# Performance work log

Hardware: AMD Instinct MI355X
Metric: run time of the kernel (lower is better)

The kernel has to match this reference:

```python
import jax, jax.numpy as jnp
import numpy as np

B, T, I, H = 64, 1024, 256, 256

def setup_inputs() -> dict:
    key = jax.random.key(0)
    ks = jax.random.split(key, 7)
    inputs = jax.random.normal(ks[0], (B * T, I), jnp.float32)
    states = jax.random.normal(ks[1], (B, 1, H), jnp.float32)  # [B, num_layers, H]
    mask = (jax.random.uniform(ks[2], (B, T, 1, 1)) < 0.9).astype(jnp.float32)
    s = 1.0 / np.sqrt(H)  # PyTorch RNN init scale
    W_ih = jax.random.uniform(ks[3], (3 * H, I), jnp.float32, -s, s)
    W_hh = jax.random.uniform(ks[4], (3 * H, H), jnp.float32, -s, s)
    b_ih = jax.random.uniform(ks[5], (3 * H,), jnp.float32, -s, s)
    b_hh = jax.random.uniform(ks[6], (3 * H,), jnp.float32, -s, s)
    return dict(inputs=inputs, states=states, mask=mask,
                W_ih=W_ih, W_hh=W_hh, b_ih=b_ih, b_hh=b_hh, seq_len=T)

def reference(inputs, states, mask, W_ih, W_hh, b_ih, b_hh, seq_len):
    # inputs: [B*T, I] -> [B, T, I]
    x = inputs.reshape(-1, seq_len, inputs.shape[-1])
    m = mask[..., 0, 0]                      # [B, T]
    # pre-loop blend: hs = states * mask[:, 0]
    h0 = states[:, 0, :] * m[:, 0:1]         # [B, H]
    xs = jnp.swapaxes(x, 0, 1)               # [T, B, I]
    ms = jnp.swapaxes(m, 0, 1)[..., None]    # [T, B, 1]

    def step(h, xm):
        x_t, m_t = xm
        gi = x_t @ W_ih.T + b_ih             # [B, 3H]
        gh = h @ W_hh.T + b_hh               # [B, 3H]
        ir, iz, i_n = jnp.split(gi, 3, axis=-1)
        hr, hz, h_n = jnp.split(gh, 3, axis=-1)
        r = jax.nn.sigmoid(ir + hr)
        z = jax.nn.sigmoid(iz + hz)
        n = jnp.tanh(i_n + r * h_n)
        nh = (1.0 - z) * n + z * h           # GRU new hidden = step output
        h_new = h * (1.0 - m_t) + nh * m_t   # masked state blend
        return h_new, nh

    h_fin, ys = jax.lax.scan(step, h0, (xs, ms))
    x_out = jnp.swapaxes(ys, 0, 1).reshape(-1, ys.shape[-1])  # [B*T, H]
    state_out = h_fin[:, None, :]                              # [B, 1, H]
    return (x_out, state_out)
```

## Files before the change

kernel.cpp:

```cpp
#include <hip/hip_runtime.h>

typedef unsigned int u32;
typedef unsigned long long u64;
typedef __fp16 f16;
typedef __fp16 h2 __attribute__((ext_vector_type(2)));
typedef __fp16 h8 __attribute__((ext_vector_type(8)));
typedef float f32x2v __attribute__((ext_vector_type(2)));
typedef float f32x4v __attribute__((ext_vector_type(4)));
typedef float f32x16v __attribute__((ext_vector_type(16)));
typedef u32 u32x2v __attribute__((ext_vector_type(2)));
typedef u32 u32x4v __attribute__((ext_vector_type(4)));

static constexpr int BB = 64;
static constexpr int TT = 1024;
static constexpr int HH = 256;
static constexpr int GG = 768;
static constexpr size_t GI_BYTES = (size_t)BB * TT * GG * 2;

__device__ __forceinline__ u32 pk2(float a, float b) {
  h2 r = __builtin_amdgcn_cvt_pkrtz(a, b);
  return __builtin_bit_cast(u32, r);
}
__device__ __forceinline__ float dpp_x1(float x) {
  return __builtin_bit_cast(float,
      __builtin_amdgcn_mov_dpp(__builtin_bit_cast(int, x), 0xB1, 0xF, 0xF, true));
}
__device__ __forceinline__ float sigf(float x) { return 1.f / (1.f + __expf(-x)); }
__device__ __forceinline__ float tanhf2(float x) {
  float e = __expf(2.f * x);
  return 1.f - 2.f / (e + 1.f);
}

__global__ void prepack_whh(const float* __restrict__ Whh, u32* __restrict__ Wp2) {
  int id = blockIdx.x * 256 + threadIdx.x;
  int j = id / 192;
  int rem = id - j * 192;
  int G = rem >> 6, d = rem & 63;
  int u = j >> 1, kh = j & 1;
  const float* p = Whh + (size_t)(G * 256 + u) * HH + 128 * kh + 2 * d;
  Wp2[id] = pk2(p[0], p[1]);
}

__device__ __forceinline__ f32x16v zero16() {
  f32x16v z;
#pragma unroll
  for (int i = 0; i < 16; ++i) z[i] = 0.f;
  return z;
}

__global__ __launch_bounds__(256, 2) void gemm_gi(
    const float* __restrict__ x, const float* __restrict__ Wih,
    const float* __restrict__ bih, const float* __restrict__ bhh,
    f16* __restrict__ gi) {
  __shared__ u32 bl[16384];
  const int tid = threadIdx.x;
  const int lane = tid & 63;
  const int wv = tid >> 6;
  const int wr = wv >> 1, wc = wv & 1;
  const int l31 = lane & 31, lh = lane >> 5;
  const int m0 = blockIdx.x << 7;

  u32x4v afr[2][16];
#pragma unroll
  for (int fr = 0; fr < 2; ++fr) {
#pragma unroll
    for (int km = 0; km < 16; ++km) {
      int row = m0 + wr * 64 + fr * 32 + l31;
      int k0 = km * 16 + lh * 8;
      const f32x4v* p = (const f32x4v*)(x + (size_t)row * 256 + k0);
      f32x4v u = p[0], v = p[1];
      u32x4v t;
      t.x = pk2(u.x, u.y); t.y = pk2(u.z, u.w);
      t.z = pk2(v.x, v.y); t.w = pk2(v.z, v.w);
      afr[fr][km] = t;
    }
  }

  for (int nt = 0; nt < 6; ++nt) {
    const int n0 = nt << 7;
#pragma unroll
    for (int it = 0; it < 32; ++it) {
      int flat = it * 256 + tid;
      int r = flat >> 6;
      int q = flat & 63;
      f32x4v f = *(const f32x4v*)(Wih + (size_t)(n0 + r) * 256 + 4 * q);
      u32x2v pw;
      pw.x = pk2(f.x, f.y);
      pw.y = pk2(f.z, f.w);
      int wd = 2 * q;
      *(u32x2v*)&bl[r * 128 + (wd ^ ((r & 15) << 2))] = pw;
    }
    __syncthreads();

    f32x16v acc00 = zero16(), acc01 = zero16(), acc10 = zero16(), acc11 = zero16();
#pragma unroll
    for (int km = 0; km < 16; ++km) {
      int w0 = km * 8 + lh * 4;
      int rc0 = wc * 64 + l31;
      int rc1 = wc * 64 + 32 + l31;
      u32x4v b0 = *(const u32x4v*)&bl[rc0 * 128 + (w0 ^ ((rc0 & 15) << 2))];
      u32x4v b1 = *(const u32x4v*)&bl[rc1 * 128 + (w0 ^ ((rc1 & 15) << 2))];
      h8 a0h = __builtin_bit_cast(h8, afr[0][km]);
      h8 a1h = __builtin_bit_cast(h8, afr[1][km]);
      h8 b0h = __builtin_bit_cast(h8, b0);
      h8 b1h = __builtin_bit_cast(h8, b1);
      acc00 = __builtin_amdgcn_mfma_f32_32x32x16_f16(a0h, b0h, acc00, 0, 0, 0);
      acc10 = __builtin_amdgcn_mfma_f32_32x32x16_f16(a1h, b0h, acc10, 0, 0, 0);
      acc01 = __builtin_amdgcn_mfma_f32_32x32x16_f16(a0h, b1h, acc01, 0, 0, 0);
      acc11 = __builtin_amdgcn_mfma_f32_32x32x16_f16(a1h, b1h, acc11, 0, 0, 0);
    }

#define EPI(ACC, FR, FC)                                                      \
    {                                                                         \
      int gc = n0 + wc * 64 + (FC) * 32 + l31;                                \
      float bias = bih[gc] + (gc < 512 ? bhh[gc] : 0.f);                      \
      _Pragma("unroll")                                                       \
      for (int rg = 0; rg < 16; ++rg) {                                       \
        int gr = m0 + wr * 64 + (FR) * 32 + 4 * lh + (rg & 3) + 8 * (rg >> 2);\
        gi[(size_t)gr * 768 + gc] = (f16)(ACC[rg] + bias);                    \
      }                                                                       \
    }
    EPI(acc00, 0, 0) EPI(acc10, 1, 0) EPI(acc01, 0, 1) EPI(acc11, 1, 1)
#undef EPI
    __syncthreads();
  }
}

#define WCLOB_LD \
  "v64","v65","v66","v67","v68","v69","v70","v71", \
  "v72","v73","v74","v75","v76","v77","v78","v79", \
  "v80","v81","v82","v83","v84","v85","v86","v87", \
  "v88","v89","v90","v91","v92","v93","v94","v95", \
  "v96","v97","v98","v99","v100","v101","v102","v103", \
  "v104","v105","v106","v107","v108","v109","v110","v111", \
  "v112","v113","v114","v115","v116","v117","v118","v119", \
  "v120","v121","v122","v123","v124","v125","v126","v127", \
  "v128","v129","v130","v131","v132","v133","v134","v135", \
  "v136","v137","v138","v139","v140","v141","v142","v143", \
  "v144","v145","v146","v147","v148","v149","v150","v151", \
  "v152","v153","v154","v155","v156","v157","v158","v159", \
  "v160","v161","v162","v163","v164","v165","v166","v167", \
  "v168","v169","v170","v171","v172","v173","v174","v175", \
  "v176","v177","v178","v179","v180","v181","v182","v183", \
  "v184","v185","v186","v187","v188","v189","v190","v191", \
  "v192","v193","v194","v195","v196","v197","v198","v199", \
  "v200","v201","v202","v203","v204","v205","v206","v207", \
  "v208","v209","v210","v211","v212","v213","v214","v215", \
  "v216","v217","v218","v219","v220","v221","v222","v223", \
  "v224","v225","v226","v227","v228","v229","v230","v231", \
  "v232","v233","v234","v235","v236","v237","v238","v239", \
  "v240","v241","v242","v243","v244","v245","v246","v247", \
  "v248","v249","v250","v251","v252","v253","v254","v255"

#define WCLOB "v56","v57","v58","v59","v60","v61","v62","v63", WCLOB_LD

#define LD16(A,B,OFF) "global_load_dwordx4 v[" #A ":" #B "], %0, off offset:" #OFF "\n\t"

#define RD_A(OFF) "ds_read_b128 v[56:59], %3 offset:" #OFF "\n\t"
#define RD_B(OFF) "ds_read_b128 v[60:63], %3 offset:" #OFF "\n\t"
#define WT1 "s_waitcnt lgkmcnt(1)\n\t"
#define WT0 "s_waitcnt lgkmcnt(0)\n\t"

#define GRP(Q0,Q1,Q2,Q3, R0,R1,R2,R3, Z0,Z1,Z2,Z3, N0,N1,N2,N3) \
  "v_dot2_f32_f16 %0, v" #R0 ", v" #Q0 ", %0\n\t" \
  "v_dot2_f32_f16 %1, v" #Z0 ", v" #Q0 ", %1\n\t" \
  "v_dot2_f32_f16 %2, v" #N0 ", v" #Q0 ", %2\n\t" \
  "v_dot2_f32_f16 %0, v" #R1 ", v" #Q1 ", %0\n\t" \
  "v_dot2_f32_f16 %1, v" #Z1 ", v" #Q1 ", %1\n\t" \
  "v_dot2_f32_f16 %2, v" #N1 ", v" #Q1 ", %2\n\t" \
  "v_dot2_f32_f16 %0, v" #R2 ", v" #Q2 ", %0\n\t" \
  "v_dot2_f32_f16 %1, v" #Z2 ", v" #Q2 ", %1\n\t" \
  "v_dot2_f32_f16 %2, v" #N2 ", v" #Q2 ", %2\n\t" \
  "v_dot2_f32_f16 %0, v" #R3 ", v" #Q3 ", %0\n\t" \
  "v_dot2_f32_f16 %1, v" #Z3 ", v" #Q3 ", %1\n\t" \
  "v_dot2_f32_f16 %2, v" #N3 ", v" #Q3 ", %2\n\t"

__global__ __launch_bounds__(512, 2) void recur(
    const u32* __restrict__ Wp2, const f16* __restrict__ gi,
    const float* __restrict__ states, const float* __restrict__ mask,
    const float* __restrict__ bhh_g, float* __restrict__ out) {
  const int b = blockIdx.x;
  const int j = threadIdx.x;
  const int u = j >> 1;
  const int kh = j & 1;

  __shared__ __align__(16) u32 hbuf[2][128];
  __shared__ float mlds[TT];

  const float bhn = bhh_g[512 + u];

  const float* mk = mask + b * TT;
  const f16* gcur = gi + (size_t)b * TT * GG + u;
  float* outb = out + (size_t)b * TT * HH;

  for (int i = j; i < TT; i += 512) mlds[i] = mk[i];

  float hreg = states[b * HH + u] * mk[0];
  if (kh == 0) ((f16*)hbuf[0])[u] = (f16)hreg;

  {
    u64 wa = (u64)(Wp2 + (size_t)j * 192);
    asm volatile(
      LD16(64,67,0)    LD16(68,71,16)   LD16(72,75,32)   LD16(76,79,48)
      LD16(80,83,64)   LD16(84,87,80)   LD16(88,91,96)   LD16(92,95,112)
      LD16(96,99,128)  LD16(100,103,144) LD16(104,107,160) LD16(108,111,176)
      LD16(112,115,192) LD16(116,119,208) LD16(120,123,224) LD16(124,127,240)
      LD16(128,131,256) LD16(132,135,272) LD16(136,139,288) LD16(140,143,304)
      LD16(144,147,320) LD16(148,151,336) LD16(152,155,352) LD16(156,159,368)
      LD16(160,163,384) LD16(164,167,400) LD16(168,171,416) LD16(172,175,432)
      LD16(176,179,448) LD16(180,183,464) LD16(184,187,480) LD16(188,191,496)
      LD16(192,195,512) LD16(196,199,528) LD16(200,203,544) LD16(204,207,560)
      LD16(208,211,576) LD16(212,215,592) LD16(216,219,608) LD16(220,223,624)
      LD16(224,227,640) LD16(228,231,656) LD16(232,235,672) LD16(236,239,688)
      LD16(240,243,704) LD16(244,247,720) LD16(248,251,736) LD16(252,255,752)
      "s_waitcnt vmcnt(0)\n\t"
      :: "v"(wa) : WCLOB_LD, "memory");
  }
  __syncthreads();

  float nh_prev = 0.f;

  for (int t = 0; t < TT; ++t) {
    if (t > 0 && kh == 0) outb[(size_t)(t - 1) * HH + u] = nh_prev;
    f16 gr_c = gcur[0], gz_c = gcur[256], gn_c = gcur[512];

    u32 lds_addr = (u32)(size_t)(&hbuf[t & 1][kh << 6]);
    float ar = 0.f, az = 0.f, an = 0.f;

    asm volatile(
      WT0
      RD_A(0) RD_B(16)
      WT1 GRP(56,57,58,59,  64,65,66,67,    128,129,130,131, 192,193,194,195) RD_A(32)
      WT1 GRP(60,61,62,63,  68,69,70,71,    132,133,134,135, 196,197,198,199) RD_B(48)
      WT1 GRP(56,57,58,59,  72,73,74,75,    136,137,138,139, 200,201,202,203) RD_A(64)
      WT1 GRP(60,61,62,63,  76,77,78,79,    140,141,142,143, 204,205,206,207) RD_B(80)
      WT1 GRP(56,57,58,59,  80,81,82,83,    144,145,146,147, 208,209,210,211) RD_A(96)
      WT1 GRP(60,61,62,63,  84,85,86,87,    148,149,150,151, 212,213,214,215) RD_B(112)
      WT1 GRP(56,57,58,59,  88,89,90,91,    152,153,154,155, 216,217,218,219) RD_A(128)
      WT1 GRP(60,61,62,63,  92,93,94,95,    156,157,158,159, 220,221,222,223) RD_B(144)
      WT1 GRP(56,57,58,59,  96,97,98,99,    160,161,162,163, 224,225,226,227) RD_A(160)
      WT1 GRP(60,61,62,63,  100,101,102,103, 164,165,166,167, 228,229,230,231) RD_B(176)
      WT1 GRP(56,57,58,59,  104,105,106,107, 168,169,170,171, 232,233,234,235) RD_A(192)
      WT1 GRP(60,61,62,63,  108,109,110,111, 172,173,174,175, 236,237,238,239) RD_B(208)
      WT1 GRP(56,57,58,59,  112,113,114,115, 176,177,178,179, 240,241,242,243) RD_A(224)
      WT1 GRP(60,61,62,63,  116,117,118,119, 180,181,182,183, 244,245,246,247) RD_B(240)
      WT1 GRP(56,57,58,59,  120,121,122,123, 184,185,186,187, 248,249,250,251)
      WT0 GRP(60,61,62,63,  124,125,126,127, 188,189,190,191, 252,253,254,255)
      : "+v"(ar), "+v"(az), "+v"(an)
      : "v"(lds_addr)
      : WCLOB, "memory");

    const float mt = mlds[t];

    float ghr = ar + dpp_x1(ar);
    float ghz = az + dpp_x1(az);
    float ghn = an + dpp_x1(an);

    float r = sigf((float)gr_c + ghr);
    float z = sigf((float)gz_c + ghz);
    float n = tanhf2((float)gn_c + r * (ghn + bhn));
    float nh = z * (hreg - n) + n;
    float hnew = hreg + mt * (nh - hreg);
    nh_prev = nh;
    hreg = hnew;
    if (kh == 0) ((f16*)hbuf[(t + 1) & 1])[u] = (f16)hnew;
    gcur += GG;
    __syncthreads();
  }

  if (kh == 0) {
    outb[(size_t)(TT - 1) * HH + u] = nh_prev;
    out[(size_t)BB * TT * HH + b * HH + u] = hreg;
  }
}

extern "C" void kernel_launch(void* const* d_in, const int* in_sizes, int n_in,
                              void* d_out, int out_size, void* d_ws, size_t ws_size,
                              hipStream_t stream) {
  const float* x      = (const float*)d_in[0];
  const float* states = (const float*)d_in[1];
  const float* mask   = (const float*)d_in[2];
  const float* W_ih   = (const float*)d_in[3];
  const float* W_hh   = (const float*)d_in[4];
  const float* b_ih   = (const float*)d_in[5];
  const float* b_hh   = (const float*)d_in[6];
  float* out = (float*)d_out;

  char* ws = (char*)d_ws;
  f16* gi = (f16*)ws;
  u32* Wp2 = (u32*)(ws + GI_BYTES);

  prepack_whh<<<dim3(384), dim3(256), 0, stream>>>(W_hh, Wp2);
  gemm_gi<<<dim3(512), dim3(256), 0, stream>>>(x, W_ih, b_ih, b_hh, gi);
  recur<<<dim3(64), dim3(512), 0, stream>>>(Wp2, gi, states, mask, b_hh, out);
}
```

Before: 1.298 ms.

## Remap GRU recurrence so each thread computes two rows over a quarter of K

The recurrent kernel now assigns each thread two hidden units and a quarter of the K dimension, instead of one unit and half of K. Each hidden-state value read from LDS then feeds six dot products rather than three, halving LDS reads per FLOP, and four read buffers are kept in flight. The hidden buffer is padded per K-chunk to avoid bank conflicts, and W_hh is prepacked to match the new layout. The cost is a two-step DPP reduction across four lanes and duplicated gate math per thread.

```diff
diff --git a/kernel.cpp b/kernel.cpp
--- a/kernel.cpp
+++ b/kernel.cpp
@@ -25,6 +25,15 @@
   return __builtin_bit_cast(float,
       __builtin_amdgcn_mov_dpp(__builtin_bit_cast(int, x), 0xB1, 0xF, 0xF, true));
 }
+__device__ __forceinline__ float dpp_x2(float x) {
+  return __builtin_bit_cast(float,
+      __builtin_amdgcn_mov_dpp(__builtin_bit_cast(int, x), 0x4E, 0xF, 0xF, true));
+}
+__device__ __forceinline__ float qred(float x) {
+  x += dpp_x1(x);
+  x += dpp_x2(x);
+  return x;
+}
 __device__ __forceinline__ float sigf(float x) { return 1.f / (1.f + __expf(-x)); }
 __device__ __forceinline__ float tanhf2(float x) {
   float e = __expf(2.f * x);
@@ -34,10 +43,16 @@
 __global__ void prepack_whh(const float* __restrict__ Whh, u32* __restrict__ Wp2) {
   int id = blockIdx.x * 256 + threadIdx.x;
   int j = id / 192;
-  int rem = id - j * 192;
-  int G = rem >> 6, d = rem & 63;
-  int u = j >> 1, kh = j & 1;
-  const float* p = Whh + (size_t)(G * 256 + u) * HH + 128 * kh + 2 * d;
+  int i = id - j * 192;
+  int m = i / 24;
+  int r24 = i - m * 24;
+  int e = r24 / 6;
+  int rs = r24 - e * 6;
+  int G = rs >> 1, uu = rs & 1;
+  int rg = j >> 2, kc = j & 3;
+  int row = G * 256 + 2 * rg + uu;
+  int k = 64 * kc + 8 * m + 2 * e;
+  const float* p = Whh + (size_t)row * HH + k;
   Wp2[id] = pk2(p[0], p[1]);
 }
 
@@ -152,28 +167,28 @@
   "v240","v241","v242","v243","v244","v245","v246","v247", \
   "v248","v249","v250","v251","v252","v253","v254","v255"
 
-#define WCLOB "v56","v57","v58","v59","v60","v61","v62","v63", WCLOB_LD
+#define WCLOB \
+  "v48","v49","v50","v51","v52","v53","v54","v55", \
+  "v56","v57","v58","v59","v60","v61","v62","v63", WCLOB_LD
 
 #define LD16(A,B,OFF) "global_load_dwordx4 v[" #A ":" #B "], %0, off offset:" #OFF "\n\t"
 
-#define RD_A(OFF) "ds_read_b128 v[56:59], %3 offset:" #OFF "\n\t"
-#define RD_B(OFF) "ds_read_b128 v[60:63], %3 offset:" #OFF "\n\t"
+#define RD0(OFF) "ds_read_b128 v[48:51], %6 offset:" #OFF "\n\t"
+#define RD1(OFF) "ds_read_b128 v[52:55], %6 offset:" #OFF "\n\t"
+#define RD2(OFF) "ds_read_b128 v[56:59], %6 offset:" #OFF "\n\t"
+#define RD3(OFF) "ds_read_b128 v[60:63], %6 offset:" #OFF "\n\t"
+#define WT3 "s_waitcnt lgkmcnt(3)\n\t"
+#define WT2 "s_waitcnt lgkmcnt(2)\n\t"
 #define WT1 "s_waitcnt lgkmcnt(1)\n\t"
 #define WT0 "s_waitcnt lgkmcnt(0)\n\t"
 
-#define GRP(Q0,Q1,Q2,Q3, R0,R1,R2,R3, Z0,Z1,Z2,Z3, N0,N1,N2,N3) \
-  "v_dot2_f32_f16 %0, v" #R0 ", v" #Q0 ", %0\n\t" \
-  "v_dot2_f32_f16 %1, v" #Z0 ", v" #Q0 ", %1\n\t" \
-  "v_dot2_f32_f16 %2, v" #N0 ", v" #Q0 ", %2\n\t" \
-  "v_dot2_f32_f16 %0, v" #R1 ", v" #Q1 ", %0\n\t" \
-  "v_dot2_f32_f16 %1, v" #Z1 ", v" #Q1 ", %1\n\t" \
-  "v_dot2_f32_f16 %2, v" #N1 ", v" #Q1 ", %2\n\t" \
-  "v_dot2_f32_f16 %0, v" #R2 ", v" #Q2 ", %0\n\t" \
-  "v_dot2_f32_f16 %1, v" #Z2 ", v" #Q2 ", %1\n\t" \
-  "v_dot2_f32_f16 %2, v" #N2 ", v" #Q2 ", %2\n\t" \
-  "v_dot2_f32_f16 %0, v" #R3 ", v" #Q3 ", %0\n\t" \
-  "v_dot2_f32_f16 %1, v" #Z3 ", v" #Q3 ", %1\n\t" \
-  "v_dot2_f32_f16 %2, v" #N3 ", v" #Q3 ", %2\n\t"
+#define D6(Q, W0,W1,W2,W3,W4,W5) \
+  "v_dot2_f32_f16 %0, v" #W0 ", v" #Q ", %0\n\t" \
+  "v_dot2_f32_f16 %1, v" #W1 ", v" #Q ", %1\n\t" \
+  "v_dot2_f32_f16 %2, v" #W2 ", v" #Q ", %2\n\t" \
+  "v_dot2_f32_f16 %3, v" #W3 ", v" #Q ", %3\n\t" \
+  "v_dot2_f32_f16 %4, v" #W4 ", v" #Q ", %4\n\t" \
+  "v_dot2_f32_f16 %5, v" #W5 ", v" #Q ", %5\n\t"
 
 __global__ __launch_bounds__(512, 2) void recur(
     const u32* __restrict__ Wp2, const f16* __restrict__ gi,
@@ -181,22 +196,28 @@
     const float* __restrict__ bhh_g, float* __restrict__ out) {
   const int b = blockIdx.x;
   const int j = threadIdx.x;
-  const int u = j >> 1;
-  const int kh = j & 1;
-
-  __shared__ __align__(16) u32 hbuf[2][128];
+  const int rg = j >> 2;
+  const int kc = j & 3;
+  const int u2 = 2 * rg;
+
+  __shared__ __align__(16) u32 hbuf[2][144];
   __shared__ float mlds[TT];
 
-  const float bhn = bhh_g[512 + u];
+  const f32x2v bn2 = *(const f32x2v*)(bhh_g + 512 + u2);
 
   const float* mk = mask + b * TT;
-  const f16* gcur = gi + (size_t)b * TT * GG + u;
+  const f16* gcur = gi + (size_t)b * TT * GG;
   float* outb = out + (size_t)b * TT * HH;
 
   for (int i = j; i < TT; i += 512) mlds[i] = mk[i];
 
-  float hreg = states[b * HH + u] * mk[0];
-  if (kh == 0) ((f16*)hbuf[0])[u] = (f16)hreg;
+  const float mk0 = mk[0];
+  float hreg0 = states[b * HH + u2] * mk0;
+  float hreg1 = states[b * HH + u2 + 1] * mk0;
+  if (j < 256) {
+    float hv = states[b * HH + j] * mk0;
+    ((f16*)hbuf[0])[(j >> 6) * 72 + (j & 63)] = (f16)hv;
+  }
 
   {
     u64 wa = (u64)(Wp2 + (size_t)j * 192);
@@ -218,59 +239,85 @@
   }
   __syncthreads();
 
-  float nh_prev = 0.f;
+  float nh_prev0 = 0.f, nh_prev1 = 0.f;
 
   for (int t = 0; t < TT; ++t) {
-    if (t > 0 && kh == 0) outb[(size_t)(t - 1) * HH + u] = nh_prev;
-    f16 gr_c = gcur[0], gz_c = gcur[256], gn_c = gcur[512];
-
-    u32 lds_addr = (u32)(size_t)(&hbuf[t & 1][kh << 6]);
-    float ar = 0.f, az = 0.f, an = 0.f;
+    if (t > 0 && kc == 0) {
+      f32x2v o; o.x = nh_prev0; o.y = nh_prev1;
+      *(f32x2v*)(outb + (size_t)(t - 1) * HH + u2) = o;
+    }
+    const f16* gt = gcur + (size_t)t * GG;
+    h2 g_r = *(const h2*)(gt + u2);
+    h2 g_z = *(const h2*)(gt + 256 + u2);
+    h2 g_n = *(const h2*)(gt + 512 + u2);
+
+    u32 lds_addr = (u32)(size_t)(&hbuf[t & 1][0]) + kc * 144;
+    float ar0 = 0.f, ar1 = 0.f, az0 = 0.f, az1 = 0.f, an0 = 0.f, an1 = 0.f;
 
     asm volatile(
       WT0
-      RD_A(0) RD_B(16)
-      WT1 GRP(56,57,58,59,  64,65,66,67,    128,129,130,131, 192,193,194,195) RD_A(32)
-      WT1 GRP(60,61,62,63,  68,69,70,71,    132,133,134,135, 196,197,198,199) RD_B(48)
-      WT1 GRP(56,57,58,59,  72,73,74,75,    136,137,138,139, 200,201,202,203) RD_A(64)
-      WT1 GRP(60,61,62,63,  76,77,78,79,    140,141,142,143, 204,205,206,207) RD_B(80)
-      WT1 GRP(56,57,58,59,  80,81,82,83,    144,145,146,147, 208,209,210,211) RD_A(96)
-      WT1 GRP(60,61,62,63,  84,85,86,87,    148,149,150,151, 212,213,214,215) RD_B(112)
-      WT1 GRP(56,57,58,59,  88,89,90,91,    152,153,154,155, 216,217,218,219) RD_A(128)
-      WT1 GRP(60,61,62,63,  92,93,94,95,    156,157,158,159, 220,221,222,223) RD_B(144)
-      WT1 GRP(56,57,58,59,  96,97,98,99,    160,161,162,163, 224,225,226,227) RD_A(160)
-      WT1 GRP(60,61,62,63,  100,101,102,103, 164,165,166,167, 228,229,230,231) RD_B(176)
-      WT1 GRP(56,57,58,59,  104,105,106,107, 168,169,170,171, 232,233,234,235) RD_A(192)
-      WT1 GRP(60,61,62,63,  108,109,110,111, 172,173,174,175, 236,237,238,239) RD_B(208)
-      WT1 GRP(56,57,58,59,  112,113,114,115, 176,177,178,179, 240,241,242,243) RD_A(224)
-      WT1 GRP(60,61,62,63,  116,117,118,119, 180,181,182,183, 244,245,246,247) RD_B(240)
-      WT1 GRP(56,57,58,59,  120,121,122,123, 184,185,186,187, 248,249,250,251)
-      WT0 GRP(60,61,62,63,  124,125,126,127, 188,189,190,191, 252,253,254,255)
-      : "+v"(ar), "+v"(az), "+v"(an)
+      RD0(0) RD1(16) RD2(32) RD3(48)
+      WT3
+      D6(48, 64,65,66,67,68,69) D6(49, 70,71,72,73,74,75)
+      D6(50, 76,77,78,79,80,81) D6(51, 82,83,84,85,86,87)
+      RD0(64)
+      WT3
+      D6(52, 88,89,90,91,92,93) D6(53, 94,95,96,97,98,99)
+      D6(54, 100,101,102,103,104,105) D6(55, 106,107,108,109,110,111)
+      RD1(80)
+      WT3
+      D6(56, 112,113,114,115,116,117) D6(57, 118,119,120,121,122,123)
+      D6(58, 124,125,126,127,128,129) D6(59, 130,131,132,133,134,135)
+      RD2(96)
+      WT3
+      D6(60, 136,137,138,139,140,141) D6(61, 142,143,144,145,146,147)
+      D6(62, 148,149,150,151,152,153) D6(63, 154,155,156,157,158,159)
+      RD3(112)
+      WT3
+      D6(48, 160,161,162,163,164,165) D6(49, 166,167,168,169,170,171)
+      D6(50, 172,173,174,175,176,177) D6(51, 178,179,180,181,182,183)
+      WT2
+      D6(52, 184,185,186,187,188,189) D6(53, 190,191,192,193,194,195)
+      D6(54, 196,197,198,199,200,201) D6(55, 202,203,204,205,206,207)
+      WT1
+      D6(56, 208,209,210,211,212,213) D6(57, 214,215,216,217,218,219)
+      D6(58, 220,221,222,223,224,225) D6(59, 226,227,228,229,230,231)
+      WT0
+      D6(60, 232,233,234,235,236,237) D6(61, 238,239,240,241,242,243)
+      D6(62, 244,245,246,247,248,249) D6(63, 250,251,252,253,254,255)
+      : "+v"(ar0), "+v"(ar1), "+v"(az0), "+v"(az1), "+v"(an0), "+v"(an1)
       : "v"(lds_addr)
       : WCLOB, "memory");
 
     const float mt = mlds[t];
 
-    float ghr = ar + dpp_x1(ar);
-    float ghz = az + dpp_x1(az);
-    float ghn = an + dpp_x1(an);
-
-    float r = sigf((float)gr_c + ghr);
-    float z = sigf((float)gz_c + ghz);
-    float n = tanhf2((float)gn_c + r * (ghn + bhn));
-    float nh = z * (hreg - n) + n;
-    float hnew = hreg + mt * (nh - hreg);
-    nh_prev = nh;
-    hreg = hnew;
-    if (kh == 0) ((f16*)hbuf[(t + 1) & 1])[u] = (f16)hnew;
-    gcur += GG;
+    float ghr0 = qred(ar0), ghr1 = qred(ar1);
+    float ghz0 = qred(az0), ghz1 = qred(az1);
+    float ghn0 = qred(an0), ghn1 = qred(an1);
+
+    float r0 = sigf((float)g_r[0] + ghr0);
+    float z0 = sigf((float)g_z[0] + ghz0);
+    float n0 = tanhf2((float)g_n[0] + r0 * (ghn0 + bn2.x));
+    float nh0 = z0 * (hreg0 - n0) + n0;
+    hreg0 = hreg0 + mt * (nh0 - hreg0);
+
+    float r1 = sigf((float)g_r[1] + ghr1);
+    float z1 = sigf((float)g_z[1] + ghz1);
+    float n1 = tanhf2((float)g_n[1] + r1 * (ghn1 + bn2.y));
+    float nh1 = z1 * (hreg1 - n1) + n1;
+    hreg1 = hreg1 + mt * (nh1 - hreg1);
+
+    nh_prev0 = nh0; nh_prev1 = nh1;
+    if (kc == 0)
+      hbuf[(t + 1) & 1][(rg >> 5) * 36 + (rg & 31)] = pk2(hreg0, hreg1);
     __syncthreads();
   }
 
-  if (kh == 0) {
-    outb[(size_t)(TT - 1) * HH + u] = nh_prev;
-    out[(size_t)BB * TT * HH + b * HH + u] = hreg;
+  if (kc == 0) {
+    f32x2v o; o.x = nh_prev0; o.y = nh_prev1;
+    *(f32x2v*)(outb + (size_t)(TT - 1) * HH + u2) = o;
+    f32x2v hf; hf.x = hreg0; hf.y = hreg1;
+    *(f32x2v*)(out + (size_t)BB * TT * HH + (size_t)b * HH + u2) = hf;
   }
 }
 
```

Measured after the change: 1.491 ms. +14.8%, slower.
